# Kernel optimization log

Hardware: AMD Instinct MI355X
Metric: run time of the kernel (lower is better)

The kernel has to match this reference:

```python
import jax, jax.numpy as jnp
import numpy as np

N, E, B, D, NODE_DIM, REL = 50000, 800000, 500, 64, 6, 200
IN_FEAT = 3 * D + 2 * NODE_DIM  # 204


def _xavier(k, shape):
    fan_out, fan_in = shape
    lim = float(np.sqrt(6.0 / (fan_in + fan_out)))
    return jax.random.uniform(k, shape, jnp.float32, -lim, lim)


def setup_inputs() -> dict:
    key = jax.random.key(0)
    ks = jax.random.split(key, 8)
    x = jax.random.normal(ks[0], (N, NODE_DIM), jnp.float32)
    edge_index = jax.random.randint(ks[1], (2, E), 0, N, jnp.int32)
    edge_rel = jax.random.randint(ks[2], (E,), 0, REL, jnp.int32)
    batch = jnp.repeat(jnp.arange(B, dtype=jnp.int32), N // B)  # 100 nodes/graph
    mask = jnp.ones((E,), jnp.float32)
    edge_emb = jax.random.normal(ks[3], (REL, D), jnp.float32) * 0.02
    W0 = _xavier(ks[4], (D, IN_FEAT))
    W1 = _xavier(ks[5], (D, IN_FEAT))
    W2 = _xavier(ks[6], (D, IN_FEAT))
    b0 = jnp.zeros((D,), jnp.float32)
    b1 = jnp.zeros((D,), jnp.float32)
    b2 = jnp.zeros((D,), jnp.float32)
    return {"x": x, "edge_index": edge_index, "edge_rel": edge_rel, "batch": batch,
            "mask": mask, "edge_emb": edge_emb, "W0": W0, "b0": b0, "W1": W1,
            "b1": b1, "W2": W2, "b2": b2, "num_graphs": B}


def reference(x, edge_index, edge_rel, batch, mask, edge_emb, W0, b0, W1, b1, W2, b2, num_graphs):
    n_nodes = x.shape[0]
    row, col = edge_index[0], edge_index[1]
    # head/tail idxs: cumulative offsets of per-graph node counts
    num_per = jax.ops.segment_sum(jnp.ones_like(batch, jnp.float32), batch, num_segments=num_graphs)
    head_idxs = jnp.cumsum(jnp.concatenate([jnp.zeros(1, jnp.float32), num_per[:-1]])).astype(jnp.int32)
    tail_idxs = head_idxs + 1
    # zero x except head/tail rows
    x0 = jnp.zeros_like(x).at[head_idxs].set(x[head_idxs]).at[tail_idxs].set(x[tail_idxs])
    ea = edge_emb[edge_rel]  # [E, D]
    m = mask[:, None]
    for W, b in ((W0, b0), (W1, b1), (W2, b2)):
        agg = jax.ops.segment_sum(ea * m, col, num_segments=n_nodes)  # [N, D]
        cnt = jax.ops.segment_sum(m, col, num_segments=n_nodes)      # [N, 1]
        node_rep = jnp.concatenate([agg / (cnt + 1.0), x0], axis=1)  # [N, D+6]
        edge_rep = jnp.concatenate([node_rep[row], node_rep[col], ea], axis=-1)  # [E, 204]
        ea = jax.nn.relu(edge_rep @ W.T + b)  # PathCon edge_mlp + gnn_non_linear
    agg = jax.ops.segment_sum(ea * m, col, num_segments=n_nodes)
    cnt = jax.ops.segment_sum(m, col, num_segments=n_nodes)
    node_rep = agg / (cnt + 1.0)  # [N, D]
    pooled = jax.ops.segment_max(node_rep, batch, num_segments=num_graphs)  # 'max' readout
    graph_emb = jnp.concatenate([pooled, node_rep[head_idxs], node_rep[tail_idxs]], axis=1)
    return graph_emb, node_rep, ea
```

## Files before the change

### kernel.cpp

```cpp
#include <hip/hip_runtime.h>
#include <stdint.h>

typedef __attribute__((ext_vector_type(8))) short short8;
typedef __attribute__((ext_vector_type(4))) float f32x4;
typedef __attribute__((ext_vector_type(2))) float f32x2;
typedef __attribute__((ext_vector_type(2))) unsigned int u32x2;

#define D_ 64
#define NODE_DIM_ 6
#define INF_ 204
#define NF_STRIDE 72
#define EB 64
#define WEA_PER_LAYER 4096
#define WN_PER_LAYER 12288

__device__ __forceinline__ unsigned int f2bf(float f){
  uint32_t u = __float_as_uint(f);
  u += 0x7fffu + ((u >> 16) & 1u);
  return u >> 16;
}

__global__ void k_count_batch(const int* __restrict__ batch, int* __restrict__ counts, int n){
  int i = blockIdx.x*256 + threadIdx.x;
  if (i < n) atomicAdd(&counts[batch[i]], 1);
}

__global__ void k_scan_heads(const int* __restrict__ counts, int* __restrict__ head, int B){
  __shared__ int s[1024];
  int t = threadIdx.x;
  int v = (t < B) ? counts[t] : 0;
  s[t] = v;
  __syncthreads();
  for (int off = 1; off < 1024; off <<= 1){
    int u = (t >= off) ? s[t-off] : 0;
    __syncthreads();
    s[t] += u;
    __syncthreads();
  }
  if (t < B) head[t] = s[t] - v;
}

__global__ void k_cnt_int(const int* __restrict__ col, int* __restrict__ cnt, int E){
  int e = blockIdx.x*256 + threadIdx.x;
  if (e < E) atomicAdd(&cnt[col[e]], 1);
}

__global__ void k_scan_off(const int* __restrict__ cnt, int* __restrict__ off, int Nn){
  __shared__ int s[1024];
  int t = threadIdx.x;
  const int CH = (Nn + 1024) / 1024;
  int base = t*CH;
  int sum = 0;
  for (int i = 0; i < CH; ++i){ int idx = base+i; if (idx < Nn) sum += cnt[idx]; }
  s[t] = sum;
  __syncthreads();
  for (int o = 1; o < 1024; o <<= 1){
    int u = (t >= o) ? s[t-o] : 0;
    __syncthreads();
    s[t] += u;
    __syncthreads();
  }
  int run = (t == 0) ? 0 : s[t-1];
  for (int i = 0; i < CH; ++i){
    int idx = base+i;
    if (idx <= Nn){ off[idx] = run; if (idx < Nn) run += cnt[idx]; }
  }
}

__global__ void k_fill(const int* __restrict__ row, const int* __restrict__ col,
                       const int* __restrict__ rel, const float* __restrict__ mask,
                       const int* __restrict__ off, int* __restrict__ fpos,
                       int* __restrict__ csr, int* __restrict__ rowp, int* __restrict__ colp,
                       int* __restrict__ relp, float* __restrict__ maskp, int E){
  int e = blockIdx.x*256 + threadIdx.x;
  if (e >= E) return;
  int c = col[e];
  int p = atomicAdd(&fpos[c], 1);
  int pos = off[c] + p;
  csr[pos]  = e;
  rowp[pos] = row[e];
  colp[pos] = c;
  relp[pos] = rel[e];
  maskp[pos]= mask[e];
}

__global__ void k_x0(const int* __restrict__ head, const float* __restrict__ x,
                     float* __restrict__ nf, int B){
  int idx = blockIdx.x*256 + threadIdx.x;
  if (idx >= B*2*NODE_DIM_) return;
  int g = idx / (2*NODE_DIM_);
  int j = idx % (2*NODE_DIM_);
  int node = head[g] + j / NODE_DIM_;
  int c = j % NODE_DIM_;
  nf[(size_t)node*NF_STRIDE + D_ + c] = x[node*NODE_DIM_ + c];
}

__global__ void k_pack_w(const float* __restrict__ W0, const float* __restrict__ W1,
                         const float* __restrict__ W2,
                         unsigned short* __restrict__ Wea, unsigned short* __restrict__ Wn){
  int idx = blockIdx.x*256 + threadIdx.x;
  if (idx < 3*WEA_PER_LAYER){
    int l = idx / WEA_PER_LAYER;
    int rem = idx % WEA_PER_LAYER;
    const float* W = (l==0) ? W0 : ((l==1) ? W1 : W2);
    int i = rem & 7, s = rem >> 3;
    int lane = s & 63, t = s >> 6;
    int kc = t & 1, nt = t >> 1;
    int n = lane & 15, kg = lane >> 4;
    int k = kc*32 + kg*8 + i;
    int c = nt*16 + n;
    Wea[idx] = (unsigned short)f2bf(W[c*INF_ + 140 + k]);
    return;
  }
  int idx2 = idx - 3*WEA_PER_LAYER;
  if (idx2 >= 3*WN_PER_LAYER) return;
  int l = idx2 / WN_PER_LAYER;
  int rem = idx2 % WN_PER_LAYER;
  const float* W = (l==0) ? W0 : ((l==1) ? W1 : W2);
  int i = rem & 7, s = rem >> 3;
  int lane = s & 63, t = s >> 6;
  int kc = t % 3, nt = t / 3;
  int n = lane & 15, kg = lane >> 4;
  int k = kc*32 + kg*8 + i;
  int c = nt*16 + n;
  float v = 0.f;
  if (k < 70) v = (nt < 4) ? W[c*INF_ + k] : W[(c-64)*INF_ + 70 + k];
  Wn[idx2] = (unsigned short)f2bf(v);
}

__global__ void k_pack_emb(const float* __restrict__ emb, unsigned short* __restrict__ emb_bf, int n){
  int i = blockIdx.x*256 + threadIdx.x;
  if (i < n) emb_bf[i] = (unsigned short)f2bf(emb[i]);
}

__global__ __launch_bounds__(256) void k_agg_seq(
    const unsigned short* __restrict__ eap, const int* __restrict__ off,
    const float* __restrict__ maskp, float* __restrict__ outp,
    int ostride, int Nn)
{
  int wid = (blockIdx.x*256 + threadIdx.x) >> 6;
  if (wid >= Nn) return;
  int lane = threadIdx.x & 63;
  int sub = lane >> 4, q = lane & 15;
  int s = off[wid], t = off[wid+1];
  float a0=0.f,a1=0.f,a2=0.f,a3=0.f, cs=0.f;
  for (int i = s; i < t; i += 4){
    int ii = i + sub;
    float mv = (ii < t) ? maskp[ii] : 0.f;
    int ie = (ii < t) ? ii : s;
    u32x2 u = *reinterpret_cast<const u32x2*>(&eap[(size_t)ie*D_ + q*4]);
    a0 += __uint_as_float(u.x << 16) * mv;
    a1 += __uint_as_float(u.x & 0xffff0000u) * mv;
    a2 += __uint_as_float(u.y << 16) * mv;
    a3 += __uint_as_float(u.y & 0xffff0000u) * mv;
    cs += mv;
  }
  a0 += __shfl_xor(a0,16); a1 += __shfl_xor(a1,16); a2 += __shfl_xor(a2,16);
  a3 += __shfl_xor(a3,16); cs += __shfl_xor(cs,16);
  a0 += __shfl_xor(a0,32); a1 += __shfl_xor(a1,32); a2 += __shfl_xor(a2,32);
  a3 += __shfl_xor(a3,32); cs += __shfl_xor(cs,32);
  if (sub == 0){
    float inv = 1.f/(cs + 1.f);
    f32x4 w = {a0*inv, a1*inv, a2*inv, a3*inv};
    *reinterpret_cast<f32x4*>(&outp[(size_t)wid*ostride + q*4]) = w;
  }
}

__global__ __launch_bounds__(256) void k_agg0_seq(
    const float* __restrict__ emb, const int* __restrict__ relp,
    const int* __restrict__ off, const float* __restrict__ maskp,
    float* __restrict__ nf, int Nn)
{
  int wid = (blockIdx.x*256 + threadIdx.x) >> 6;
  if (wid >= Nn) return;
  int lane = threadIdx.x & 63;
  int sub = lane >> 4, q = lane & 15;
  int s = off[wid], t = off[wid+1];
  float a0=0.f,a1=0.f,a2=0.f,a3=0.f, cs=0.f;
  for (int i = s; i < t; i += 4){
    int ii = i + sub;
    float mv = (ii < t) ? maskp[ii] : 0.f;
    int r = (ii < t) ? relp[ii] : 0;
    f32x4 v = *reinterpret_cast<const f32x4*>(&emb[r*D_ + q*4]);
    a0 += v.x*mv; a1 += v.y*mv; a2 += v.z*mv; a3 += v.w*mv;
    cs += mv;
  }
  a0 += __shfl_xor(a0,16); a1 += __shfl_xor(a1,16); a2 += __shfl_xor(a2,16);
  a3 += __shfl_xor(a3,16); cs += __shfl_xor(cs,16);
  a0 += __shfl_xor(a0,32); a1 += __shfl_xor(a1,32); a2 += __shfl_xor(a2,32);
  a3 += __shfl_xor(a3,32); cs += __shfl_xor(cs,32);
  if (sub == 0){
    float inv = 1.f/(cs + 1.f);
    f32x4 w = {a0*inv, a1*inv, a2*inv, a3*inv};
    *reinterpret_cast<f32x4*>(&nf[(size_t)wid*NF_STRIDE + q*4]) = w;
  }
}

__global__ __launch_bounds__(256) void k_ynode(
    const float* __restrict__ nf, const unsigned short* __restrict__ Wn,
    const float* __restrict__ bias, float* __restrict__ Ybuf, int Nn)
{
  __shared__ __align__(16) short tile[32*104];
  int tid = threadIdx.x;
  int n0 = blockIdx.x*32;
  if (tid < 128){
    int e = tid >> 2, w = tid & 3;
    *reinterpret_cast<short8*>(&tile[e*104 + 72 + w*8]) = short8{0,0,0,0,0,0,0,0};
  }
  const f32x4* nf4 = reinterpret_cast<const f32x4*>(nf);
  for (int s = tid; s < 32*18; s += 256){
    int e = s/18, q = s - e*18;
    f32x4 v = {0.f,0.f,0.f,0.f};
    if (n0 + e < Nn) v = nf4[(size_t)(n0+e)*18 + q];
    u32x2 pk;
    pk.x = f2bf(v.x) | (f2bf(v.y) << 16);
    pk.y = f2bf(v.z) | (f2bf(v.w) << 16);
    *reinterpret_cast<u32x2*>(&tile[e*104 + q*4]) = pk;
  }
  __syncthreads();
  int lane = tid & 63, wv = tid >> 6;
  int r16 = lane & 15, kg = lane >> 4;
  const short8* W8 = reinterpret_cast<const short8*>(Wn);
  f32x4 acc[2][2] = {};
  #pragma unroll
  for (int kc = 0; kc < 3; ++kc){
    short8 a0 = *reinterpret_cast<const short8*>(&tile[r16*104 + kc*32 + kg*8]);
    short8 a1 = *reinterpret_cast<const short8*>(&tile[(16+r16)*104 + kc*32 + kg*8]);
    #pragma unroll
    for (int t = 0; t < 2; ++t){
      int nt = wv*2 + t;
      short8 wf = W8[(nt*3 + kc)*64 + lane];
      acc[0][t] = __builtin_amdgcn_mfma_f32_16x16x32_bf16(a0, wf, acc[0][t], 0,0,0);
      acc[1][t] = __builtin_amdgcn_mfma_f32_16x16x32_bf16(a1, wf, acc[1][t], 0,0,0);
    }
  }
  #pragma unroll
  for (int t = 0; t < 2; ++t){
    int nt = wv*2 + t;
    int c = nt*16 + r16;
    float b = (nt < 4) ? bias[c] : 0.f;
    #pragma unroll
    for (int m = 0; m < 2; ++m)
      #pragma unroll
      for (int j = 0; j < 4; ++j){
        int node = n0 + m*16 + kg*4 + j;
        if (node < Nn) Ybuf[(size_t)node*128 + c] = acc[m][t][j] + b;
      }
  }
}

template<int FIRST, int FOUT>
__global__ __launch_bounds__(256) void k_gemm(
    const unsigned short* __restrict__ ea_bf, const unsigned short* __restrict__ emb_bf,
    const float* __restrict__ Ybuf,
    unsigned short* __restrict__ ea_out_bf, float* __restrict__ ea_out_f32,
    const int* __restrict__ rowp, const int* __restrict__ colp,
    const int* __restrict__ relp, const int* __restrict__ csr,
    const unsigned short* __restrict__ Wea, int E)
{
  __shared__ __align__(16) float stile[EB*68];
  __shared__ int s_row[EB], s_col[EB], s_rel[EB], s_csr[EB];
  int tid = threadIdx.x;
  int e0 = blockIdx.x*EB;
  if (tid < EB){
    int ge = e0 + tid;
    bool ok = ge < E;
    s_row[tid] = ok ? rowp[ge] : 0;
    s_col[tid] = ok ? colp[ge] : 0;
    s_rel[tid] = (FIRST && ok) ? relp[ge] : 0;
    s_csr[tid] = (FOUT && ok) ? csr[ge] : 0;
  }
  __syncthreads();
  const f32x4* Yb4 = reinterpret_cast<const f32x4*>(Ybuf);
  f32x4* st4 = reinterpret_cast<f32x4*>(stile);
  #pragma unroll
  for (int h = 0; h < 4; ++h){
    int s = tid + h*256;
    int e = s >> 4, q = s & 15;
    f32x4 a = Yb4[(size_t)s_row[e]*32 + q];
    f32x4 b = Yb4[(size_t)s_col[e]*32 + 16 + q];
    st4[e*17 + q] = a + b;
  }
  int lane = tid & 63, wv = tid >> 6;
  int r16 = lane & 15, kg = lane >> 4;
  const short8* W8 = reinterpret_cast<const short8*>(Wea);
  short8 wf[4][2];
  #pragma unroll
  for (int nt = 0; nt < 4; ++nt)
    #pragma unroll
    for (int kc = 0; kc < 2; ++kc)
      wf[nt][kc] = W8[(nt*2 + kc)*64 + lane];
  f32x4 acc[4] = {};
  #pragma unroll
  for (int kc = 0; kc < 2; ++kc){
    short8 a;
    if (FIRST){
      a = *reinterpret_cast<const short8*>(&emb_bf[(size_t)s_rel[wv*16 + r16]*D_ + kc*32 + kg*8]);
    } else {
      int eA = e0 + wv*16 + r16; if (eA >= E) eA = E-1;
      a = *reinterpret_cast<const short8*>(&ea_bf[(size_t)eA*D_ + kc*32 + kg*8]);
    }
    #pragma unroll
    for (int nt = 0; nt < 4; ++nt)
      acc[nt] = __builtin_amdgcn_mfma_f32_16x16x32_bf16(a, wf[nt][kc], acc[nt], 0,0,0);
  }
  __syncthreads();
  float v[4][4];
  #pragma unroll
  for (int nt = 0; nt < 4; ++nt)
    #pragma unroll
    for (int j = 0; j < 4; ++j){
      int et = wv*16 + kg*4 + j;
      float x = acc[nt][j] + stile[et*68 + nt*16 + r16];
      v[nt][j] = x > 0.f ? x : 0.f;
    }
  __syncthreads();
  if (FOUT == 0){
    unsigned short* ob = reinterpret_cast<unsigned short*>(stile);
    #pragma unroll
    for (int nt = 0; nt < 4; ++nt)
      #pragma unroll
      for (int j = 0; j < 4; ++j)
        ob[(wv*16 + kg*4 + j)*72 + nt*16 + r16] = (unsigned short)f2bf(v[nt][j]);
    __syncthreads();
    #pragma unroll
    for (int h = 0; h < 2; ++h){
      int s = tid + h*256;
      int e = s >> 3, w = s & 7;
      int ge = e0 + e;
      if (ge < E)
        *reinterpret_cast<short8*>(&ea_out_bf[(size_t)ge*D_ + w*8]) =
          *reinterpret_cast<const short8*>(&ob[e*72 + w*8]);
    }
  } else {
    #pragma unroll
    for (int nt = 0; nt < 4; ++nt)
      #pragma unroll
      for (int j = 0; j < 4; ++j)
        stile[(wv*16 + kg*4 + j)*68 + nt*16 + r16] = v[nt][j];
    __syncthreads();
    f32x4* out4 = reinterpret_cast<f32x4*>(ea_out_f32);
    #pragma unroll
    for (int h = 0; h < 4; ++h){
      int s = tid + h*256;
      int e = s >> 4, q = s & 15;
      int ge = e0 + e;
      if (ge < E){
        f32x4 w = st4[e*17 + q];
        out4[(size_t)s_csr[e]*16 + q] = w;
        u32x2 pk;
        pk.x = f2bf(w.x) | (f2bf(w.y) << 16);
        pk.y = f2bf(w.z) | (f2bf(w.w) << 16);
        *reinterpret_cast<u32x2*>(&ea_out_bf[(size_t)ge*D_ + q*4]) = pk;
      }
    }
  }
}

__global__ void k_pool(const float* __restrict__ nrep_out, const int* __restrict__ head,
                       const int* __restrict__ counts, float* __restrict__ gout, int B){
  __shared__ float s[4][64];
  int g = blockIdx.x;
  int lane = threadIdx.x & 63, sub = threadIdx.x >> 6;
  int h = head[g]; int n = counts[g];
  float m = -3.402823466e38f;
  for (int i = sub; i < n; i += 4)
    m = fmaxf(m, nrep_out[(size_t)(h+i)*D_ + lane]);
  s[sub][lane] = m;
  __syncthreads();
  if (sub == 0){
    m = fmaxf(fmaxf(s[0][lane], s[1][lane]), fmaxf(s[2][lane], s[3][lane]));
    gout[(size_t)g*192 + lane]       = m;
    gout[(size_t)g*192 + 64  + lane] = nrep_out[(size_t)h*D_ + lane];
    gout[(size_t)g*192 + 128 + lane] = nrep_out[(size_t)(h+1)*D_ + lane];
  }
}

extern "C" void kernel_launch(void* const* d_in, const int* in_sizes, int n_in,
                              void* d_out, int out_size, void* d_ws, size_t ws_size,
                              hipStream_t stream)
{
  const float* x    = (const float*)d_in[0];
  const int*   eidx = (const int*)d_in[1];
  const int*   erel = (const int*)d_in[2];
  const int*   batch= (const int*)d_in[3];
  const float* mask = (const float*)d_in[4];
  const float* emb  = (const float*)d_in[5];
  const float* W0   = (const float*)d_in[6];
  const float* b0   = (const float*)d_in[7];
  const float* W1   = (const float*)d_in[8];
  const float* b1   = (const float*)d_in[9];
  const float* W2   = (const float*)d_in[10];
  const float* b2   = (const float*)d_in[11];

  int N = in_sizes[0] / NODE_DIM_;
  int E = in_sizes[2];
  int B = (int)(((long long)out_size - (long long)N*D_ - (long long)E*D_) / 192);

  float* out_ge   = (float*)d_out;
  float* out_nrep = out_ge + (size_t)B*192;
  float* out_ea   = out_nrep + (size_t)N*D_;

  char* w = (char*)d_ws;
  auto alloc = [&](size_t bytes)->char*{ char* p = w; w += (bytes + 255) & ~(size_t)255; return p; };
  unsigned short* ea_p = (unsigned short*)alloc((size_t)E*D_*2);
  float* nf     = (float*)alloc((size_t)N*NF_STRIDE*4);
  float* Ybuf   = (float*)alloc((size_t)N*128*4);
  int*   cnt_i  = (int*)  alloc((size_t)N*4);
  int*   off    = (int*)  alloc((size_t)(N+1)*4);
  int*   fpos   = (int*)  alloc((size_t)N*4);
  int*   csr    = (int*)  alloc((size_t)E*4);
  int*   rowp   = (int*)  alloc((size_t)E*4);
  int*   colp   = (int*)  alloc((size_t)E*4);
  int*   relp   = (int*)  alloc((size_t)E*4);
  float* maskp  = (float*)alloc((size_t)E*4);
  int*   counts = (int*)  alloc((size_t)B*4);
  int*   head   = (int*)  alloc((size_t)B*4);
  unsigned short* Wea = (unsigned short*)alloc((size_t)3*WEA_PER_LAYER*2);
  unsigned short* Wn  = (unsigned short*)alloc((size_t)3*WN_PER_LAYER*2);
  unsigned short* emb_bf = (unsigned short*)alloc((size_t)200*D_*2 + 256);

  hipMemsetAsync(nf,     0, (size_t)N*NF_STRIDE*4, stream);
  hipMemsetAsync(cnt_i,  0, (size_t)N*4, stream);
  hipMemsetAsync(fpos,   0, (size_t)N*4, stream);
  hipMemsetAsync(counts, 0, (size_t)B*4, stream);

  const int* erow = eidx;
  const int* ecol = eidx + E;

  k_count_batch<<<(N+255)/256, 256, 0, stream>>>(batch, counts, N);
  k_scan_heads <<<1, 1024, 0, stream>>>(counts, head, B);
  k_x0         <<<(B*2*NODE_DIM_+255)/256, 256, 0, stream>>>(head, x, nf, B);
  k_cnt_int    <<<(E+255)/256, 256, 0, stream>>>(ecol, cnt_i, E);
  k_scan_off   <<<1, 1024, 0, stream>>>(cnt_i, off, N);
  k_fill       <<<(E+255)/256, 256, 0, stream>>>(erow, ecol, erel, mask, off, fpos,
                                                 csr, rowp, colp, relp, maskp, E);
  k_pack_w     <<<(3*(WEA_PER_LAYER+WN_PER_LAYER)+255)/256, 256, 0, stream>>>(W0, W1, W2, Wea, Wn);
  k_pack_emb   <<<(200*D_+255)/256, 256, 0, stream>>>(emb, emb_bf, 200*D_);

  int nblk_g = (E + EB - 1) / EB;
  int nblk_a = (N + 3) / 4;
  int nblk_y = (N + 31) / 32;

  k_agg0_seq<<<nblk_a, 256, 0, stream>>>(emb, relp, off, maskp, nf, N);
  k_ynode<<<nblk_y, 256, 0, stream>>>(nf, Wn, b0, Ybuf, N);
  k_gemm<1,0><<<nblk_g, 256, 0, stream>>>(ea_p, emb_bf, Ybuf, ea_p, out_ea,
                                          rowp, colp, relp, csr, Wea, E);
  k_agg_seq<<<nblk_a, 256, 0, stream>>>(ea_p, off, maskp, nf, NF_STRIDE, N);
  k_ynode<<<nblk_y, 256, 0, stream>>>(nf, Wn + WN_PER_LAYER, b1, Ybuf, N);
  k_gemm<0,0><<<nblk_g, 256, 0, stream>>>(ea_p, emb_bf, Ybuf, ea_p, out_ea,
                                          rowp, colp, relp, csr, Wea + WEA_PER_LAYER, E);
  k_agg_seq<<<nblk_a, 256, 0, stream>>>(ea_p, off, maskp, nf, NF_STRIDE, N);
  k_ynode<<<nblk_y, 256, 0, stream>>>(nf, Wn + 2*WN_PER_LAYER, b2, Ybuf, N);
  k_gemm<0,1><<<nblk_g, 256, 0, stream>>>(ea_p, emb_bf, Ybuf, ea_p, out_ea,
                                          rowp, colp, relp, csr, Wea + 2*WEA_PER_LAYER, E);

  k_agg_seq<<<nblk_a, 256, 0, stream>>>(ea_p, off, maskp, out_nrep, D_, N);
  k_pool<<<B, 256, 0, stream>>>(out_nrep, head, counts, out_ge, B);
}
```

Baseline: 827.8 us.

## Fuse segment-mean aggregation into edge GEMM epilogue via run-length atomics

Removes the separate per-node aggregation kernels after each edge layer. Each edge-GEMM block now accumulates its outputs, scaled by mask and a precomputed 1/(cnt+1), into the node buffer with atomicAdd, grouping consecutive CSR-sorted edges that share a column. The node features are split into a dense agg buffer and a separate x0 buffer. The count and scan kernels are merged to cut launches. The last layer also stops writing the bf16 edge copy. The cost is float atomic traffic and nondeterministic summation order, plus extra memsets between layers.

```diff
diff --git a/kernel.cpp b/kernel.cpp
--- a/kernel.cpp
+++ b/kernel.cpp
@@ -3,13 +3,11 @@
 
 typedef __attribute__((ext_vector_type(8))) short short8;
 typedef __attribute__((ext_vector_type(4))) float f32x4;
-typedef __attribute__((ext_vector_type(2))) float f32x2;
 typedef __attribute__((ext_vector_type(2))) unsigned int u32x2;
 
 #define D_ 64
 #define NODE_DIM_ 6
 #define INF_ 204
-#define NF_STRIDE 72
 #define EB 64
 #define WEA_PER_LAYER 4096
 #define WN_PER_LAYER 12288
@@ -20,32 +18,15 @@
   return u >> 16;
 }
 
-__global__ void k_count_batch(const int* __restrict__ batch, int* __restrict__ counts, int n){
+__global__ void k_counts(const int* __restrict__ batch, const int* __restrict__ col,
+                         int* __restrict__ counts, int* __restrict__ cnt, int N, int E){
   int i = blockIdx.x*256 + threadIdx.x;
-  if (i < n) atomicAdd(&counts[batch[i]], 1);
-}
-
-__global__ void k_scan_heads(const int* __restrict__ counts, int* __restrict__ head, int B){
-  __shared__ int s[1024];
-  int t = threadIdx.x;
-  int v = (t < B) ? counts[t] : 0;
-  s[t] = v;
-  __syncthreads();
-  for (int off = 1; off < 1024; off <<= 1){
-    int u = (t >= off) ? s[t-off] : 0;
-    __syncthreads();
-    s[t] += u;
-    __syncthreads();
-  }
-  if (t < B) head[t] = s[t] - v;
-}
-
-__global__ void k_cnt_int(const int* __restrict__ col, int* __restrict__ cnt, int E){
-  int e = blockIdx.x*256 + threadIdx.x;
-  if (e < E) atomicAdd(&cnt[col[e]], 1);
-}
-
-__global__ void k_scan_off(const int* __restrict__ cnt, int* __restrict__ off, int Nn){
+  if (i < E) atomicAdd(&cnt[col[i]], 1);
+  if (i < N) atomicAdd(&counts[batch[i]], 1);
+}
+
+__global__ void k_scans(const int* __restrict__ cnt, int* __restrict__ off, int Nn,
+                        const int* __restrict__ counts, int* __restrict__ head, int B){
   __shared__ int s[1024];
   int t = threadIdx.x;
   const int CH = (Nn + 1024) / 1024;
@@ -65,6 +46,17 @@
     int idx = base+i;
     if (idx <= Nn){ off[idx] = run; if (idx < Nn) run += cnt[idx]; }
   }
+  __syncthreads();
+  int v = (t < B) ? counts[t] : 0;
+  s[t] = v;
+  __syncthreads();
+  for (int o = 1; o < 1024; o <<= 1){
+    int u = (t >= o) ? s[t-o] : 0;
+    __syncthreads();
+    s[t] += u;
+    __syncthreads();
+  }
+  if (t < B) head[t] = s[t] - v;
 }
 
 __global__ void k_fill(const int* __restrict__ row, const int* __restrict__ col,
@@ -84,15 +76,15 @@
   maskp[pos]= mask[e];
 }
 
-__global__ void k_x0(const int* __restrict__ head, const float* __restrict__ x,
-                     float* __restrict__ nf, int B){
+__global__ void k_x0b(const int* __restrict__ head, const float* __restrict__ x,
+                      float* __restrict__ x0b, int B){
   int idx = blockIdx.x*256 + threadIdx.x;
   if (idx >= B*2*NODE_DIM_) return;
   int g = idx / (2*NODE_DIM_);
   int j = idx % (2*NODE_DIM_);
   int node = head[g] + j / NODE_DIM_;
   int c = j % NODE_DIM_;
-  nf[(size_t)node*NF_STRIDE + D_ + c] = x[node*NODE_DIM_ + c];
+  x0b[(size_t)node*8 + c] = x[node*NODE_DIM_ + c];
 }
 
 __global__ void k_pack_w(const float* __restrict__ W0, const float* __restrict__ W1,
@@ -133,43 +125,10 @@
   if (i < n) emb_bf[i] = (unsigned short)f2bf(emb[i]);
 }
 
-__global__ __launch_bounds__(256) void k_agg_seq(
-    const unsigned short* __restrict__ eap, const int* __restrict__ off,
-    const float* __restrict__ maskp, float* __restrict__ outp,
-    int ostride, int Nn)
-{
-  int wid = (blockIdx.x*256 + threadIdx.x) >> 6;
-  if (wid >= Nn) return;
-  int lane = threadIdx.x & 63;
-  int sub = lane >> 4, q = lane & 15;
-  int s = off[wid], t = off[wid+1];
-  float a0=0.f,a1=0.f,a2=0.f,a3=0.f, cs=0.f;
-  for (int i = s; i < t; i += 4){
-    int ii = i + sub;
-    float mv = (ii < t) ? maskp[ii] : 0.f;
-    int ie = (ii < t) ? ii : s;
-    u32x2 u = *reinterpret_cast<const u32x2*>(&eap[(size_t)ie*D_ + q*4]);
-    a0 += __uint_as_float(u.x << 16) * mv;
-    a1 += __uint_as_float(u.x & 0xffff0000u) * mv;
-    a2 += __uint_as_float(u.y << 16) * mv;
-    a3 += __uint_as_float(u.y & 0xffff0000u) * mv;
-    cs += mv;
-  }
-  a0 += __shfl_xor(a0,16); a1 += __shfl_xor(a1,16); a2 += __shfl_xor(a2,16);
-  a3 += __shfl_xor(a3,16); cs += __shfl_xor(cs,16);
-  a0 += __shfl_xor(a0,32); a1 += __shfl_xor(a1,32); a2 += __shfl_xor(a2,32);
-  a3 += __shfl_xor(a3,32); cs += __shfl_xor(cs,32);
-  if (sub == 0){
-    float inv = 1.f/(cs + 1.f);
-    f32x4 w = {a0*inv, a1*inv, a2*inv, a3*inv};
-    *reinterpret_cast<f32x4*>(&outp[(size_t)wid*ostride + q*4]) = w;
-  }
-}
-
-__global__ __launch_bounds__(256) void k_agg0_seq(
+__global__ __launch_bounds__(256) void k_agg0_inv(
     const float* __restrict__ emb, const int* __restrict__ relp,
     const int* __restrict__ off, const float* __restrict__ maskp,
-    float* __restrict__ nf, int Nn)
+    float* __restrict__ agg, float* __restrict__ inv, int Nn)
 {
   int wid = (blockIdx.x*256 + threadIdx.x) >> 6;
   if (wid >= Nn) return;
@@ -190,14 +149,16 @@
   a0 += __shfl_xor(a0,32); a1 += __shfl_xor(a1,32); a2 += __shfl_xor(a2,32);
   a3 += __shfl_xor(a3,32); cs += __shfl_xor(cs,32);
   if (sub == 0){
-    float inv = 1.f/(cs + 1.f);
-    f32x4 w = {a0*inv, a1*inv, a2*inv, a3*inv};
-    *reinterpret_cast<f32x4*>(&nf[(size_t)wid*NF_STRIDE + q*4]) = w;
+    float iv = 1.f/(cs + 1.f);
+    f32x4 w = {a0*iv, a1*iv, a2*iv, a3*iv};
+    *reinterpret_cast<f32x4*>(&agg[(size_t)wid*D_ + q*4]) = w;
+    if (q == 0) inv[wid] = iv;
   }
 }
 
 __global__ __launch_bounds__(256) void k_ynode(
-    const float* __restrict__ nf, const unsigned short* __restrict__ Wn,
+    const float* __restrict__ agg, const float* __restrict__ x0b,
+    const unsigned short* __restrict__ Wn,
     const float* __restrict__ bias, float* __restrict__ Ybuf, int Nn)
 {
   __shared__ __align__(16) short tile[32*104];
@@ -207,11 +168,15 @@
     int e = tid >> 2, w = tid & 3;
     *reinterpret_cast<short8*>(&tile[e*104 + 72 + w*8]) = short8{0,0,0,0,0,0,0,0};
   }
-  const f32x4* nf4 = reinterpret_cast<const f32x4*>(nf);
+  const f32x4* agg4 = reinterpret_cast<const f32x4*>(agg);
+  const f32x4* x0b4 = reinterpret_cast<const f32x4*>(x0b);
   for (int s = tid; s < 32*18; s += 256){
     int e = s/18, q = s - e*18;
     f32x4 v = {0.f,0.f,0.f,0.f};
-    if (n0 + e < Nn) v = nf4[(size_t)(n0+e)*18 + q];
+    if (n0 + e < Nn){
+      if (q < 16) v = agg4[(size_t)(n0+e)*16 + q];
+      else        v = x0b4[(size_t)(n0+e)*2 + (q-16)];
+    }
     u32x2 pk;
     pk.x = f2bf(v.x) | (f2bf(v.y) << 16);
     pk.y = f2bf(v.z) | (f2bf(v.w) << 16);
@@ -254,21 +219,27 @@
     const unsigned short* __restrict__ ea_bf, const unsigned short* __restrict__ emb_bf,
     const float* __restrict__ Ybuf,
     unsigned short* __restrict__ ea_out_bf, float* __restrict__ ea_out_f32,
+    float* __restrict__ agg,
     const int* __restrict__ rowp, const int* __restrict__ colp,
     const int* __restrict__ relp, const int* __restrict__ csr,
+    const float* __restrict__ maskp, const float* __restrict__ inv,
     const unsigned short* __restrict__ Wea, int E)
 {
   __shared__ __align__(16) float stile[EB*68];
   __shared__ int s_row[EB], s_col[EB], s_rel[EB], s_csr[EB];
+  __shared__ float s_mask[EB], s_inv[EB];
   int tid = threadIdx.x;
   int e0 = blockIdx.x*EB;
   if (tid < EB){
     int ge = e0 + tid;
     bool ok = ge < E;
+    int cc = ok ? colp[ge] : 0;
+    s_col[tid] = cc;
     s_row[tid] = ok ? rowp[ge] : 0;
-    s_col[tid] = ok ? colp[ge] : 0;
-    s_rel[tid] = (FIRST && ok) ? relp[ge] : 0;
-    s_csr[tid] = (FOUT && ok) ? csr[ge] : 0;
+    s_mask[tid]= ok ? maskp[ge] : 0.f;
+    s_inv[tid] = inv[cc];
+    if (FIRST) s_rel[tid] = ok ? relp[ge] : 0;
+    if (FOUT)  s_csr[tid] = ok ? csr[ge] : 0;
   }
   __syncthreads();
   const f32x4* Yb4 = reinterpret_cast<const f32x4*>(Ybuf);
@@ -332,6 +303,22 @@
         *reinterpret_cast<short8*>(&ea_out_bf[(size_t)ge*D_ + w*8]) =
           *reinterpret_cast<const short8*>(&ob[e*72 + w*8]);
     }
+    {
+      int c = tid & 63, g = tid >> 6;
+      int base = g*16;
+      int cur = s_col[base]; float civ = s_inv[base]; float run = 0.f;
+      #pragma unroll
+      for (int e = base; e < base+16; ++e){
+        int col = s_col[e];
+        if (col != cur){
+          atomicAdd(&agg[(size_t)cur*D_ + c], run*civ);
+          run = 0.f; cur = col; civ = s_inv[e];
+        }
+        float val = __uint_as_float((uint32_t)ob[e*72 + c] << 16);
+        run += val * s_mask[e];
+      }
+      atomicAdd(&agg[(size_t)cur*D_ + c], run*civ);
+    }
   } else {
     #pragma unroll
     for (int nt = 0; nt < 4; ++nt)
@@ -345,14 +332,22 @@
       int s = tid + h*256;
       int e = s >> 4, q = s & 15;
       int ge = e0 + e;
-      if (ge < E){
-        f32x4 w = st4[e*17 + q];
-        out4[(size_t)s_csr[e]*16 + q] = w;
-        u32x2 pk;
-        pk.x = f2bf(w.x) | (f2bf(w.y) << 16);
-        pk.y = f2bf(w.z) | (f2bf(w.w) << 16);
-        *reinterpret_cast<u32x2*>(&ea_out_bf[(size_t)ge*D_ + q*4]) = pk;
+      if (ge < E) out4[(size_t)s_csr[e]*16 + q] = st4[e*17 + q];
+    }
+    {
+      int c = tid & 63, g = tid >> 6;
+      int base = g*16;
+      int cur = s_col[base]; float civ = s_inv[base]; float run = 0.f;
+      #pragma unroll
+      for (int e = base; e < base+16; ++e){
+        int col = s_col[e];
+        if (col != cur){
+          atomicAdd(&agg[(size_t)cur*D_ + c], run*civ);
+          run = 0.f; cur = col; civ = s_inv[e];
+        }
+        run += stile[e*68 + c] * s_mask[e];
       }
+      atomicAdd(&agg[(size_t)cur*D_ + c], run*civ);
     }
   }
 }
@@ -404,8 +399,11 @@
   char* w = (char*)d_ws;
   auto alloc = [&](size_t bytes)->char*{ char* p = w; w += (bytes + 255) & ~(size_t)255; return p; };
   unsigned short* ea_p = (unsigned short*)alloc((size_t)E*D_*2);
-  float* nf     = (float*)alloc((size_t)N*NF_STRIDE*4);
   float* Ybuf   = (float*)alloc((size_t)N*128*4);
+  float* aggP   = (float*)alloc((size_t)N*D_*4);
+  float* aggQ   = (float*)alloc((size_t)N*D_*4);
+  float* x0b    = (float*)alloc((size_t)N*8*4);
+  float* invb   = (float*)alloc((size_t)N*4);
   int*   cnt_i  = (int*)  alloc((size_t)N*4);
   int*   off    = (int*)  alloc((size_t)(N+1)*4);
   int*   fpos   = (int*)  alloc((size_t)N*4);
@@ -420,41 +418,41 @@
   unsigned short* Wn  = (unsigned short*)alloc((size_t)3*WN_PER_LAYER*2);
   unsigned short* emb_bf = (unsigned short*)alloc((size_t)200*D_*2 + 256);
 
-  hipMemsetAsync(nf,     0, (size_t)N*NF_STRIDE*4, stream);
   hipMemsetAsync(cnt_i,  0, (size_t)N*4, stream);
   hipMemsetAsync(fpos,   0, (size_t)N*4, stream);
   hipMemsetAsync(counts, 0, (size_t)B*4, stream);
+  hipMemsetAsync(x0b,    0, (size_t)N*8*4, stream);
+  hipMemsetAsync(aggQ,   0, (size_t)N*D_*4, stream);
 
   const int* erow = eidx;
   const int* ecol = eidx + E;
 
-  k_count_batch<<<(N+255)/256, 256, 0, stream>>>(batch, counts, N);
-  k_scan_heads <<<1, 1024, 0, stream>>>(counts, head, B);
-  k_x0         <<<(B*2*NODE_DIM_+255)/256, 256, 0, stream>>>(head, x, nf, B);
-  k_cnt_int    <<<(E+255)/256, 256, 0, stream>>>(ecol, cnt_i, E);
-  k_scan_off   <<<1, 1024, 0, stream>>>(cnt_i, off, N);
-  k_fill       <<<(E+255)/256, 256, 0, stream>>>(erow, ecol, erel, mask, off, fpos,
-                                                 csr, rowp, colp, relp, maskp, E);
-  k_pack_w     <<<(3*(WEA_PER_LAYER+WN_PER_LAYER)+255)/256, 256, 0, stream>>>(W0, W1, W2, Wea, Wn);
-  k_pack_emb   <<<(200*D_+255)/256, 256, 0, stream>>>(emb, emb_bf, 200*D_);
+  k_counts   <<<(E+255)/256, 256, 0, stream>>>(batch, ecol, counts, cnt_i, N, E);
+  k_scans    <<<1, 1024, 0, stream>>>(cnt_i, off, N, counts, head, B);
+  k_x0b      <<<(B*2*NODE_DIM_+255)/256, 256, 0, stream>>>(head, x, x0b, B);
+  k_fill     <<<(E+255)/256, 256, 0, stream>>>(erow, ecol, erel, mask, off, fpos,
+                                               csr, rowp, colp, relp, maskp, E);
+  k_pack_w   <<<(3*(WEA_PER_LAYER+WN_PER_LAYER)+255)/256, 256, 0, stream>>>(W0, W1, W2, Wea, Wn);
+  k_pack_emb <<<(200*D_+255)/256, 256, 0, stream>>>(emb, emb_bf, 200*D_);
 
   int nblk_g = (E + EB - 1) / EB;
   int nblk_a = (N + 3) / 4;
   int nblk_y = (N + 31) / 32;
 
-  k_agg0_seq<<<nblk_a, 256, 0, stream>>>(emb, relp, off, maskp, nf, N);
-  k_ynode<<<nblk_y, 256, 0, stream>>>(nf, Wn, b0, Ybuf, N);
-  k_gemm<1,0><<<nblk_g, 256, 0, stream>>>(ea_p, emb_bf, Ybuf, ea_p, out_ea,
-                                          rowp, colp, relp, csr, Wea, E);
-  k_agg_seq<<<nblk_a, 256, 0, stream>>>(ea_p, off, maskp, nf, NF_STRIDE, N);
-  k_ynode<<<nblk_y, 256, 0, stream>>>(nf, Wn + WN_PER_LAYER, b1, Ybuf, N);
-  k_gemm<0,0><<<nblk_g, 256, 0, stream>>>(ea_p, emb_bf, Ybuf, ea_p, out_ea,
-                                          rowp, colp, relp, csr, Wea + WEA_PER_LAYER, E);
-  k_agg_seq<<<nblk_a, 256, 0, stream>>>(ea_p, off, maskp, nf, NF_STRIDE, N);
-  k_ynode<<<nblk_y, 256, 0, stream>>>(nf, Wn + 2*WN_PER_LAYER, b2, Ybuf, N);
-  k_gemm<0,1><<<nblk_g, 256, 0, stream>>>(ea_p, emb_bf, Ybuf, ea_p, out_ea,
-                                          rowp, colp, relp, csr, Wea + 2*WEA_PER_LAYER, E);
-
-  k_agg_seq<<<nblk_a, 256, 0, stream>>>(ea_p, off, maskp, out_nrep, D_, N);
+  k_agg0_inv<<<nblk_a, 256, 0, stream>>>(emb, relp, off, maskp, aggP, invb, N);
+  k_ynode<<<nblk_y, 256, 0, stream>>>(aggP, x0b, Wn, b0, Ybuf, N);
+  k_gemm<1,0><<<nblk_g, 256, 0, stream>>>(ea_p, emb_bf, Ybuf, ea_p, out_ea, aggQ,
+                                          rowp, colp, relp, csr, maskp, invb, Wea, E);
+  hipMemsetAsync(aggP, 0, (size_t)N*D_*4, stream);
+  k_ynode<<<nblk_y, 256, 0, stream>>>(aggQ, x0b, Wn + WN_PER_LAYER, b1, Ybuf, N);
+  k_gemm<0,0><<<nblk_g, 256, 0, stream>>>(ea_p, emb_bf, Ybuf, ea_p, out_ea, aggP,
+                                          rowp, colp, relp, csr, maskp, invb,
+                                          Wea + WEA_PER_LAYER, E);
+  hipMemsetAsync(out_nrep, 0, (size_t)N*D_*4, stream);
+  k_ynode<<<nblk_y, 256, 0, stream>>>(aggP, x0b, Wn + 2*WN_PER_LAYER, b2, Ybuf, N);
+  k_gemm<0,1><<<nblk_g, 256, 0, stream>>>(ea_p, emb_bf, Ybuf, ea_p, out_ea, out_nrep,
+                                          rowp, colp, relp, csr, maskp, invb,
+                                          Wea + 2*WEA_PER_LAYER, E);
+
   k_pool<<<B, 256, 0, stream>>>(out_nrep, head, counts, out_ge, B);
 }
```

Result: faster. 785.1 us (-5.2%).
